# Kernel tuning notes

Measured on AMD Instinct MI355X. Metric: run time of the kernel, lower is better.

## Reference

```python
import jax, jax.numpy as jnp
import numpy as np

N_POINTS = 131072
NUM_FREQS = 6
MIN_LOG2_FREQ = 0.0
MAX_LOG2_FREQ = 5.0
NUM_QUANTS = 80
NUM_FEATS = 4
NUM_CORRS = 8
STD = 1e-4


def setup_inputs() -> dict:
    key = jax.random.key(0)
    k1, k2 = jax.random.split(key)
    # points in [-1, 1] as typical normalized NeRF scene coordinates
    points = jax.random.uniform(k1, (N_POINTS, 3), jnp.float32, -1.0, 1.0)
    # QFF1.__init__: std ** (1/x_dim), qff_vector ~ randn * std'
    std = STD ** (1.0 / 3.0)
    qff_vector = jax.random.normal(
        k2, (NUM_FREQS * 2 * 3, NUM_FEATS * NUM_CORRS, NUM_QUANTS, 1), jnp.float32) * std
    freqs = (2.0 ** jnp.linspace(MIN_LOG2_FREQ, MAX_LOG2_FREQ, NUM_FREQS)).astype(jnp.float32)
    return {"points": points, "qff_vector": qff_vector, "freqs": freqs}


def _lerp_lookup(qv, enc):
    # 1D linear interpolation, equivalent to F.grid_sample(bilinear, align_corners=True)
    # on a (Q, 1) grid with x coord fixed to 0.
    # qv: (M, CR, Q) tables; enc: (M, N) coords in [-1, 1].
    Q = qv.shape[-1]
    pos = (enc + 1.0) * 0.5 * (Q - 1)            # (M, N) in [0, Q-1]
    i0 = jnp.clip(jnp.floor(pos), 0, Q - 1).astype(jnp.int32)
    i1 = jnp.minimum(i0 + 1, Q - 1)
    w = (pos - i0.astype(pos.dtype))[:, None, :]  # (M, 1, N)
    gather = jax.vmap(lambda q, i: q[:, i])       # per-row gather: (CR, Q), (N) -> (CR, N)
    v0 = gather(qv, i0)                           # (M, CR, N)
    v1 = gather(qv, i1)
    return v0 * (1.0 - w) + v1 * w


def reference(points, qff_vector, freqs):
    # points: (N, 3); qff_vector: (NF*2*3, C*R, Q, 1); freqs: (NF,)
    N = points.shape[0]
    NF = freqs.shape[0]
    CR, Q = qff_vector.shape[1], qff_vector.shape[2]
    R = NUM_CORRS
    C = CR // R
    # pos_encode: (NF, 3, N) -> stack sin/cos -> (NF*2*3, N)
    fp = points.T[None, :, :] * freqs[:, None, None]
    enc = jnp.stack((jnp.sin(fp), jnp.cos(fp)), 1).reshape(NF * 2 * 3, N)
    qv = qff_vector.reshape(NF * 2 * 3, CR, Q)
    sampled = _lerp_lookup(qv, enc)               # (NF*2*3, C*R, N)
    sampled = sampled.reshape(NF * 2, 3, C, R, N)
    # CP decomposition: product over the 3 axes, sum over rank R
    f = (sampled[:, 0] * sampled[:, 1] * sampled[:, 2]).sum(2)  # (NF*2, C, N)
    return f.reshape(NF * 2 * C, N).T             # (N, latent_dim=NF*2*C)
```

## Files before the change

### kernel.cpp

```cpp
#include <hip/hip_runtime.h>
#include <hip/hip_fp16.h>
#include <math.h>


constexpr int N_POINTS = 131072;
constexpr int NFREQ    = 6;
constexpr int QN       = 80;
constexpr int CRN      = 32;
constexpr int M_PER_F  = 6;
constexpr int ROW      = 40;
constexpr int MSTRIDE  = QN * ROW;
constexpr int TSTRIDE  = CRN * QN;
constexpr int FH       = M_PER_F * MSTRIDE;
constexpr int FH4      = FH / 8;
constexpr int NTAB     = NFREQ * M_PER_F;
constexpr int TB       = 256;
constexpr int NBLK     = N_POINTS / TB;
constexpr int DSTR     = 25;
constexpr size_t TAB_BYTES = (size_t)NTAB * MSTRIDE * 2;

typedef float f32x4 __attribute__((ext_vector_type(4)));

__global__ __launch_bounds__(256)
void qff1_prep(const float* __restrict__ qff, __half* __restrict__ wsh)
{
    int i = blockIdx.x * 256 + threadIdx.x;
    if (i >= NTAB * TSTRIDE) return;
    int T  = i / TSTRIDE;
    int r  = i - T * TSTRIDE;
    int cr = r / QN;
    int q  = r - cr * QN;
    wsh[T * MSTRIDE + q * ROW + cr] = __float2half(qff[i]);
}

__device__ __forceinline__ void qff1_core(const __half* tab,
                                          float px, float py, float pz,
                                          float freq, float acc[8])
{
    float enc[6];
    {
        float s, cc;
        __sincosf(px * freq, &s, &cc); enc[0] = s; enc[3] = cc;
        __sincosf(py * freq, &s, &cc); enc[1] = s; enc[4] = cc;
        __sincosf(pz * freq, &s, &cc); enc[2] = s; enc[5] = cc;
    }
    int b0[6], b1[6];
    __half2 w2[6];
#pragma unroll
    for (int m = 0; m < 6; ++m) {
        float pos = (enc[m] + 1.0f) * (0.5f * (float)(QN - 1));
        float fi  = floorf(pos);
        int i0    = (int)fi;
        i0 = i0 < 0 ? 0 : (i0 > QN - 1 ? QN - 1 : i0);
        int i1 = i0 + 1; if (i1 > QN - 1) i1 = QN - 1;
        w2[m] = __float2half2_rn(pos - (float)i0);
        b0[m] = m * MSTRIDE + i0 * ROW;
        b1[m] = m * MSTRIDE + i1 * ROW;
    }
#pragma unroll
    for (int s = 0; s < 2; ++s) {
#pragma unroll
        for (int jc = 0; jc < 4; ++jc) {
            __half2 Lv[3][4];
#pragma unroll
            for (int d = 0; d < 3; ++d) {
                int m = s * 3 + d;
                union { float4 v; __half2 h[4]; } A, B;
                A.v = *(const float4*)&tab[b0[m] + jc * 8];
                B.v = *(const float4*)&tab[b1[m] + jc * 8];
#pragma unroll
                for (int kk = 0; kk < 4; ++kk)
                    Lv[d][kk] = __hfma2(w2[m], __hsub2(B.h[kk], A.h[kk]), A.h[kk]);
            }
            float a = 0.0f;
#pragma unroll
            for (int kk = 0; kk < 4; ++kk) {
                float2 f0 = __half22float2(Lv[0][kk]);
                float2 f1 = __half22float2(Lv[1][kk]);
                float2 f2 = __half22float2(Lv[2][kk]);
                a += f0.x * f1.x * f2.x + f0.y * f1.y * f2.y;
            }
            acc[s * 4 + jc] = a;
        }
    }
}

__global__ __launch_bounds__(TB, 4)
void qff1_main(const float* __restrict__ points,
               const __half* __restrict__ wsh,
               const float* __restrict__ freqs,
               float4* __restrict__ out4)
{
    __shared__ __align__(16) __half  tab[FH];
    __shared__ __align__(16) __half2 dmp2[TB * DSTR];

    const int tid = threadIdx.x;
    const int n   = blockIdx.x * TB + tid;

    const float px = points[n * 3 + 0];
    const float py = points[n * 3 + 1];
    const float pz = points[n * 3 + 2];

    for (int f = 0; f < NFREQ; ++f) {
        {
            const float4* src = reinterpret_cast<const float4*>(wsh + (size_t)f * FH);
            float4* dst = reinterpret_cast<float4*>(tab);
#pragma unroll
            for (int k = 0; k < 9; ++k)
                dst[tid + k * TB] = src[tid + k * TB];
            if (tid < FH4 - 9 * TB)
                dst[tid + 9 * TB] = src[tid + 9 * TB];
        }
        __syncthreads();

        float acc[8];
        qff1_core(tab, px, py, pz, freqs[f], acc);

        dmp2[tid * DSTR + f * 4 + 0] = __floats2half2_rn(acc[0], acc[1]);
        dmp2[tid * DSTR + f * 4 + 1] = __floats2half2_rn(acc[2], acc[3]);
        dmp2[tid * DSTR + f * 4 + 2] = __floats2half2_rn(acc[4], acc[5]);
        dmp2[tid * DSTR + f * 4 + 3] = __floats2half2_rn(acc[6], acc[7]);

        __syncthreads();
    }

    const size_t base = (size_t)blockIdx.x * (TB * 12);
#pragma unroll
    for (int k = 0; k < 12; ++k) {
        int i = tid + k * TB;
        int p = i / 12;
        int c = i - p * 12;
        float2 lo = __half22float2(dmp2[p * DSTR + 2 * c]);
        float2 hi = __half22float2(dmp2[p * DSTR + 2 * c + 1]);
        f32x4 v = { lo.x, lo.y, hi.x, hi.y };
        __builtin_nontemporal_store(v, (f32x4*)&out4[base + i]);
    }
}

__global__ __launch_bounds__(512, 8)
void qff1_fallback(const float* __restrict__ points,
                   const float* __restrict__ qff,
                   const float* __restrict__ freqs,
                   float* __restrict__ out)
{
    __shared__ __align__(16) __half tab[FH];
    const int tid = threadIdx.x;
    const int f   = blockIdx.y;

    const float* tsrc = qff + (size_t)f * (M_PER_F * CRN * QN);
    __half2* lds2 = reinterpret_cast<__half2*>(tab);
    for (int idx = tid; idx < M_PER_F * QN * (CRN / 2); idx += 512) {
        int m   = idx / (QN * CRN / 2);
        int rem = idx - m * (QN * CRN / 2);
        int q   = rem >> 4;
        int cr2 = rem & 15;
        float v0 = tsrc[m * (CRN * QN) + (2 * cr2    ) * QN + q];
        float v1 = tsrc[m * (CRN * QN) + (2 * cr2 + 1) * QN + q];
        lds2[m * (MSTRIDE / 2) + q * (ROW / 2) + cr2] = __floats2half2_rn(v0, v1);
    }
    __syncthreads();

    const int n = blockIdx.x * 512 + tid;
    float acc[8];
    qff1_core(tab, points[n * 3], points[n * 3 + 1], points[n * 3 + 2],
              freqs[f], acc);

    float4* o = (float4*)(out + (size_t)n * 48 + f * 8);
    o[0] = make_float4(acc[0], acc[1], acc[2], acc[3]);
    o[1] = make_float4(acc[4], acc[5], acc[6], acc[7]);
}

extern "C" void kernel_launch(void* const* d_in, const int* in_sizes, int n_in,
                              void* d_out, int out_size, void* d_ws, size_t ws_size,
                              hipStream_t stream) {
    const float* points = (const float*)d_in[0];
    const float* qff    = (const float*)d_in[1];
    const float* freqs  = (const float*)d_in[2];
    float* out = (float*)d_out;

    if (ws_size >= TAB_BYTES) {
        __half* wsh = (__half*)d_ws;
        qff1_prep<<<dim3((NTAB * TSTRIDE + 255) / 256), dim3(256), 0, stream>>>(qff, wsh);
        qff1_main<<<dim3(NBLK), dim3(TB), 0, stream>>>(points, wsh, freqs, (float4*)out);
    } else {
        qff1_fallback<<<dim3(N_POINTS / 512, NFREQ), dim3(512), 0, stream>>>(points, qff, freqs, out);
    }
}
```

Measured before the change: 34.87 us.

## Split sin and cos halves of each point across two threads

The main kernel now uses 512 threads per block for 256 points. Each point is handled by two threads: one computes the sin-encoded half and the other the cos-encoded half of the CP lookup and product. This halves per-thread work and register pressure so more wavefronts can hide LDS latency. In exchange, every sincos is computed twice and each block has twice as many threads taking part in the barriers and table copies.

```diff
diff --git a/kernel.cpp b/kernel.cpp
--- a/kernel.cpp
+++ b/kernel.cpp
@@ -14,8 +14,9 @@
 constexpr int FH       = M_PER_F * MSTRIDE;
 constexpr int FH4      = FH / 8;
 constexpr int NTAB     = NFREQ * M_PER_F;
-constexpr int TB       = 256;
-constexpr int NBLK     = N_POINTS / TB;
+constexpr int TB       = 512;
+constexpr int PPB      = 256;
+constexpr int NBLK     = N_POINTS / PPB;
 constexpr int DSTR     = 25;
 constexpr size_t TAB_BYTES = (size_t)NTAB * MSTRIDE * 2;
 
@@ -33,69 +34,19 @@
     wsh[T * MSTRIDE + q * ROW + cr] = __float2half(qff[i]);
 }
 
-__device__ __forceinline__ void qff1_core(const __half* tab,
-                                          float px, float py, float pz,
-                                          float freq, float acc[8])
-{
-    float enc[6];
-    {
-        float s, cc;
-        __sincosf(px * freq, &s, &cc); enc[0] = s; enc[3] = cc;
-        __sincosf(py * freq, &s, &cc); enc[1] = s; enc[4] = cc;
-        __sincosf(pz * freq, &s, &cc); enc[2] = s; enc[5] = cc;
-    }
-    int b0[6], b1[6];
-    __half2 w2[6];
-#pragma unroll
-    for (int m = 0; m < 6; ++m) {
-        float pos = (enc[m] + 1.0f) * (0.5f * (float)(QN - 1));
-        float fi  = floorf(pos);
-        int i0    = (int)fi;
-        i0 = i0 < 0 ? 0 : (i0 > QN - 1 ? QN - 1 : i0);
-        int i1 = i0 + 1; if (i1 > QN - 1) i1 = QN - 1;
-        w2[m] = __float2half2_rn(pos - (float)i0);
-        b0[m] = m * MSTRIDE + i0 * ROW;
-        b1[m] = m * MSTRIDE + i1 * ROW;
-    }
-#pragma unroll
-    for (int s = 0; s < 2; ++s) {
-#pragma unroll
-        for (int jc = 0; jc < 4; ++jc) {
-            __half2 Lv[3][4];
-#pragma unroll
-            for (int d = 0; d < 3; ++d) {
-                int m = s * 3 + d;
-                union { float4 v; __half2 h[4]; } A, B;
-                A.v = *(const float4*)&tab[b0[m] + jc * 8];
-                B.v = *(const float4*)&tab[b1[m] + jc * 8];
-#pragma unroll
-                for (int kk = 0; kk < 4; ++kk)
-                    Lv[d][kk] = __hfma2(w2[m], __hsub2(B.h[kk], A.h[kk]), A.h[kk]);
-            }
-            float a = 0.0f;
-#pragma unroll
-            for (int kk = 0; kk < 4; ++kk) {
-                float2 f0 = __half22float2(Lv[0][kk]);
-                float2 f1 = __half22float2(Lv[1][kk]);
-                float2 f2 = __half22float2(Lv[2][kk]);
-                a += f0.x * f1.x * f2.x + f0.y * f1.y * f2.y;
-            }
-            acc[s * 4 + jc] = a;
-        }
-    }
-}
-
-__global__ __launch_bounds__(TB, 4)
+__global__ __launch_bounds__(TB, 2)
 void qff1_main(const float* __restrict__ points,
                const __half* __restrict__ wsh,
                const float* __restrict__ freqs,
                float4* __restrict__ out4)
 {
     __shared__ __align__(16) __half  tab[FH];
-    __shared__ __align__(16) __half2 dmp2[TB * DSTR];
+    __shared__ __align__(16) __half2 dmp2[PPB * DSTR];
 
     const int tid = threadIdx.x;
-    const int n   = blockIdx.x * TB + tid;
+    const int p   = tid & (PPB - 1);
+    const int h   = tid >> 8;
+    const int n   = blockIdx.x * PPB + p;
 
     const float px = points[n * 3 + 0];
     const float py = points[n * 3 + 1];
@@ -106,32 +57,80 @@
             const float4* src = reinterpret_cast<const float4*>(wsh + (size_t)f * FH);
             float4* dst = reinterpret_cast<float4*>(tab);
 #pragma unroll
-            for (int k = 0; k < 9; ++k)
-                dst[tid + k * TB] = src[tid + k * TB];
-            if (tid < FH4 - 9 * TB)
-                dst[tid + 9 * TB] = src[tid + 9 * TB];
+            for (int k = 0; k < 5; ++k) {
+                int idx = tid + k * TB;
+                if (idx < FH4) dst[idx] = src[idx];
+            }
         }
         __syncthreads();
 
-        float acc[8];
-        qff1_core(tab, px, py, pz, freqs[f], acc);
-
-        dmp2[tid * DSTR + f * 4 + 0] = __floats2half2_rn(acc[0], acc[1]);
-        dmp2[tid * DSTR + f * 4 + 1] = __floats2half2_rn(acc[2], acc[3]);
-        dmp2[tid * DSTR + f * 4 + 2] = __floats2half2_rn(acc[4], acc[5]);
-        dmp2[tid * DSTR + f * 4 + 3] = __floats2half2_rn(acc[6], acc[7]);
+        const float freq = freqs[f];
+
+        float ee[3];
+        {
+            float s0, c0, s1, c1, s2, c2;
+            __sincosf(px * freq, &s0, &c0);
+            __sincosf(py * freq, &s1, &c1);
+            __sincosf(pz * freq, &s2, &c2);
+            ee[0] = h ? c0 : s0;
+            ee[1] = h ? c1 : s1;
+            ee[2] = h ? c2 : s2;
+        }
+
+        int b0[3], b1[3];
+        __half2 w2[3];
+#pragma unroll
+        for (int d = 0; d < 3; ++d) {
+            float pos = (ee[d] + 1.0f) * (0.5f * (float)(QN - 1));
+            float fi  = floorf(pos);
+            int i0    = (int)fi;
+            i0 = i0 < 0 ? 0 : (i0 > QN - 1 ? QN - 1 : i0);
+            int i1 = i0 + 1; if (i1 > QN - 1) i1 = QN - 1;
+            w2[d] = __float2half2_rn(pos - (float)i0);
+            int m = h * 3 + d;
+            b0[d] = m * MSTRIDE + i0 * ROW;
+            b1[d] = m * MSTRIDE + i1 * ROW;
+        }
+
+        float acc[4];
+#pragma unroll
+        for (int jc = 0; jc < 4; ++jc) {
+            __half2 Lv[3][4];
+#pragma unroll
+            for (int d = 0; d < 3; ++d) {
+                union { float4 v; __half2 hh[4]; } A, B;
+                A.v = *(const float4*)&tab[b0[d] + jc * 8];
+                B.v = *(const float4*)&tab[b1[d] + jc * 8];
+#pragma unroll
+                for (int kk = 0; kk < 4; ++kk)
+                    Lv[d][kk] = __hfma2(w2[d], __hsub2(B.hh[kk], A.hh[kk]), A.hh[kk]);
+            }
+            float a = 0.0f;
+#pragma unroll
+            for (int kk = 0; kk < 4; ++kk) {
+                float2 f0 = __half22float2(Lv[0][kk]);
+                float2 f1 = __half22float2(Lv[1][kk]);
+                float2 f2 = __half22float2(Lv[2][kk]);
+                a += f0.x * f1.x * f2.x + f0.y * f1.y * f2.y;
+            }
+            acc[jc] = a;
+        }
+
+        dmp2[p * DSTR + h * 12 + f * 2 + 0] = __floats2half2_rn(acc[0], acc[1]);
+        dmp2[p * DSTR + h * 12 + f * 2 + 1] = __floats2half2_rn(acc[2], acc[3]);
 
         __syncthreads();
     }
 
-    const size_t base = (size_t)blockIdx.x * (TB * 12);
-#pragma unroll
-    for (int k = 0; k < 12; ++k) {
-        int i = tid + k * TB;
-        int p = i / 12;
-        int c = i - p * 12;
-        float2 lo = __half22float2(dmp2[p * DSTR + 2 * c]);
-        float2 hi = __half22float2(dmp2[p * DSTR + 2 * c + 1]);
+    const size_t base = (size_t)blockIdx.x * (PPB * 12);
+#pragma unroll
+    for (int k = 0; k < 6; ++k) {
+        int i  = tid + k * TB;
+        int pp = i / 12;
+        int c  = i - pp * 12;
+        int off = (c & 1) * 12 + (c >> 1) * 2;
+        float2 lo = __half22float2(dmp2[pp * DSTR + off + 0]);
+        float2 hi = __half22float2(dmp2[pp * DSTR + off + 1]);
         f32x4 v = { lo.x, lo.y, hi.x, hi.y };
         __builtin_nontemporal_store(v, (f32x4*)&out4[base + i]);
     }
@@ -161,13 +160,61 @@
     __syncthreads();
 
     const int n = blockIdx.x * 512 + tid;
-    float acc[8];
-    qff1_core(tab, points[n * 3], points[n * 3 + 1], points[n * 3 + 2],
-              freqs[f], acc);
-
+    const float px = points[n * 3 + 0];
+    const float py = points[n * 3 + 1];
+    const float pz = points[n * 3 + 2];
+    const float freq = freqs[f];
+
+    float enc[6];
+    {
+        float s, cc;
+        __sincosf(px * freq, &s, &cc); enc[0] = s; enc[3] = cc;
+        __sincosf(py * freq, &s, &cc); enc[1] = s; enc[4] = cc;
+        __sincosf(pz * freq, &s, &cc); enc[2] = s; enc[5] = cc;
+    }
+    int b0[6], b1[6];
+    __half2 w2[6];
+#pragma unroll
+    for (int m = 0; m < 6; ++m) {
+        float pos = (enc[m] + 1.0f) * (0.5f * (float)(QN - 1));
+        float fi  = floorf(pos);
+        int i0    = (int)fi;
+        i0 = i0 < 0 ? 0 : (i0 > QN - 1 ? QN - 1 : i0);
+        int i1 = i0 + 1; if (i1 > QN - 1) i1 = QN - 1;
+        w2[m] = __float2half2_rn(pos - (float)i0);
+        b0[m] = m * MSTRIDE + i0 * ROW;
+        b1[m] = m * MSTRIDE + i1 * ROW;
+    }
+    float accv[8];
+#pragma unroll
+    for (int s = 0; s < 2; ++s) {
+#pragma unroll
+        for (int jc = 0; jc < 4; ++jc) {
+            __half2 Lv[3][4];
+#pragma unroll
+            for (int d = 0; d < 3; ++d) {
+                int m = s * 3 + d;
+                union { float4 v; __half2 hh[4]; } A, B;
+                A.v = *(const float4*)&tab[b0[m] + jc * 8];
+                B.v = *(const float4*)&tab[b1[m] + jc * 8];
+#pragma unroll
+                for (int kk = 0; kk < 4; ++kk)
+                    Lv[d][kk] = __hfma2(w2[m], __hsub2(B.hh[kk], A.hh[kk]), A.hh[kk]);
+            }
+            float a = 0.0f;
+#pragma unroll
+            for (int kk = 0; kk < 4; ++kk) {
+                float2 f0 = __half22float2(Lv[0][kk]);
+                float2 f1 = __half22float2(Lv[1][kk]);
+                float2 f2 = __half22float2(Lv[2][kk]);
+                a += f0.x * f1.x * f2.x + f0.y * f1.y * f2.y;
+            }
+            accv[s * 4 + jc] = a;
+        }
+    }
     float4* o = (float4*)(out + (size_t)n * 48 + f * 8);
-    o[0] = make_float4(acc[0], acc[1], acc[2], acc[3]);
-    o[1] = make_float4(acc[4], acc[5], acc[6], acc[7]);
+    o[0] = make_float4(accv[0], accv[1], accv[2], accv[3]);
+    o[1] = make_float4(accv[4], accv[5], accv[6], accv[7]);
 }
 
 extern "C" void kernel_launch(void* const* d_in, const int* in_sizes, int n_in,
```

Result: faster. 33.25 us (-4.7%).
